# Kernel optimization log

Measured on AMD Instinct MI355X. Metric: run time of the kernel, lower is better.

## Reference

```python
import jax, jax.numpy as jnp
import numpy as np

N = 50000          # nodes (ogbn-products-like subgraph)
E = 800000         # directed edges (avg degree 16)
F_IN, HID, HEADS, OUT = 100, 32, 4, 47
W1 = HID * HEADS   # 128
NEG_SLOPE = 0.2
BN_EPS = 1e-5


def _gatv2(x, src, dst, w_src, w_dst, att, bias, heads, ch):
    """GATv2Conv (PyG semantics, share_weights=False, concat).
    x: [N, F]; src/dst: [Etot] (self-loops already appended);
    w_src/w_dst: [F, heads*ch]; att: [heads, ch]; bias: [heads*ch].
    """
    n = x.shape[0]
    xl = (x @ w_src).reshape(n, heads, ch)   # source-side transform
    xr = (x @ w_dst).reshape(n, heads, ch)   # target-side transform
    # per-edge attention logits: a . leaky_relu(xl[j] + xr[i])  -> [E, heads]
    e = jnp.sum(jax.nn.leaky_relu(xl[src] + xr[dst], NEG_SLOPE) * att, axis=-1)
    # segment softmax over incoming edges of each destination node
    m = jax.ops.segment_max(e, dst, num_segments=n)          # [N, heads]
    ex = jnp.exp(e - m[dst])
    denom = jax.ops.segment_sum(ex, dst, num_segments=n)     # [N, heads]
    alpha = ex / denom[dst]                                  # [E, heads]
    # weighted scatter-add aggregation of source features
    out = jax.ops.segment_sum(alpha[:, :, None] * xl[src], dst, num_segments=n)
    return out.reshape(n, heads * ch) + bias


def _bn_eval(x, g, b, m, v):
    return (x - m) * jax.lax.rsqrt(v + BN_EPS) * g + b


def setup_inputs() -> dict:
    key = jax.random.key(0)
    ks = jax.random.split(key, 32)
    s = 0.1
    inp = {
        "x": jax.random.normal(ks[0], (N, F_IN), jnp.float32),
        "edge_index": jax.random.randint(ks[1], (2, E), 0, N, dtype=jnp.int32),
        "w1_src": jax.random.normal(ks[2], (F_IN, W1), jnp.float32) * s,
        "w1_dst": jax.random.normal(ks[3], (F_IN, W1), jnp.float32) * s,
        "att1": jax.random.normal(ks[4], (HEADS, HID), jnp.float32) * s,
        "b1": jnp.zeros((W1,), jnp.float32),
        "bn1_g": jnp.ones((W1,), jnp.float32),
        "bn1_b": jnp.zeros((W1,), jnp.float32),
        "bn1_m": jax.random.normal(ks[5], (W1,), jnp.float32) * 0.05,
        "bn1_v": jax.random.uniform(ks[6], (W1,), jnp.float32, 0.5, 1.5),
        "res0_w": jax.random.normal(ks[7], (F_IN, W1), jnp.float32) * s,
        "res0_b": jnp.zeros((W1,), jnp.float32),
        "w2_src": jax.random.normal(ks[8], (W1, W1), jnp.float32) * s,
        "w2_dst": jax.random.normal(ks[9], (W1, W1), jnp.float32) * s,
        "att2": jax.random.normal(ks[10], (HEADS, HID), jnp.float32) * s,
        "b2": jnp.zeros((W1,), jnp.float32),
        "bn2_g": jnp.ones((W1,), jnp.float32),
        "bn2_b": jnp.zeros((W1,), jnp.float32),
        "bn2_m": jax.random.normal(ks[11], (W1,), jnp.float32) * 0.05,
        "bn2_v": jax.random.uniform(ks[12], (W1,), jnp.float32, 0.5, 1.5),
        # layer 3: 128 -> 47, heads=1
        "w3_src": jax.random.normal(ks[13], (W1, OUT), jnp.float32) * s,
        "w3_dst": jax.random.normal(ks[14], (W1, OUT), jnp.float32) * s,
        "att3": jax.random.normal(ks[15], (1, OUT), jnp.float32) * s,
        "b3": jnp.zeros((OUT,), jnp.float32),
        "bn3_g": jnp.ones((OUT,), jnp.float32),
        "bn3_b": jnp.zeros((OUT,), jnp.float32),
        "bn3_m": jax.random.normal(ks[16], (OUT,), jnp.float32) * 0.05,
        "bn3_v": jax.random.uniform(ks[17], (OUT,), jnp.float32, 0.5, 1.5),
        "res2_w": jax.random.normal(ks[18], (W1, OUT), jnp.float32) * s,
        "res2_b": jnp.zeros((OUT,), jnp.float32),
    }
    return inp


def reference(x, edge_index,
              w1_src, w1_dst, att1, b1, bn1_g, bn1_b, bn1_m, bn1_v, res0_w, res0_b,
              w2_src, w2_dst, att2, b2, bn2_g, bn2_b, bn2_m, bn2_v,
              w3_src, w3_dst, att3, b3, bn3_g, bn3_b, bn3_m, bn3_v, res2_w, res2_b):
    # add self-loops (PyG GATv2Conv default add_self_loops=True)
    loops = jnp.arange(x.shape[0], dtype=edge_index.dtype)
    src = jnp.concatenate([edge_index[0], loops])
    dst = jnp.concatenate([edge_index[1], loops])

    # layer 1 + linear residual + BN + relu (eval mode: no dropout)
    h = _gatv2(x, src, dst, w1_src, w1_dst, att1, b1, HEADS, HID)
    h = h + (x @ res0_w + res0_b)
    h = jax.nn.relu(_bn_eval(h, bn1_g, bn1_b, bn1_m, bn1_v))

    # layer 2 + identity residual + BN + relu
    h2 = _gatv2(h, src, dst, w2_src, w2_dst, att2, b2, HEADS, HID)
    h2 = h2 + h
    h2 = jax.nn.relu(_bn_eval(h2, bn2_g, bn2_b, bn2_m, bn2_v))

    # layer 3 (heads=1) + linear residual + BN (no relu/dropout on last layer)
    out = _gatv2(h2, src, dst, w3_src, w3_dst, att3, b3, 1, OUT)
    out = out + (h2 @ res2_w + res2_b)
    out = _bn_eval(out, bn3_g, bn3_b, bn3_m, bn3_v)
    return out
```

## Files before the change

### kernel.cpp

```cpp
#include <hip/hip_runtime.h>
#include <math.h>

#define BN_EPS 1e-5f
#define SLOT 96
#define LN16 2.7725887f
#define BCAP 5120

typedef _Float16 h2 __attribute__((ext_vector_type(2)));
typedef _Float16 h4 __attribute__((ext_vector_type(4)));
typedef _Float16 h8 __attribute__((ext_vector_type(8)));
typedef float f2v __attribute__((ext_vector_type(2)));
typedef float float4v __attribute__((ext_vector_type(4)));

static __device__ inline h2 bit_h2(unsigned u) {
    union { unsigned u; h2 h; } c; c.u = u; return c.h;
}
static __device__ inline unsigned bit_u(h2 h) {
    union { unsigned u; h2 h; } c; c.h = h; return c.u;
}

template <int CTRL>
static __device__ inline float dpp_add(float x) {
    int y = __builtin_amdgcn_update_dpp(0, __float_as_int(x), CTRL, 0xF, 0xF, true);
    return x + __int_as_float(y);
}
static __device__ inline float red8_dpp(float t) {
    t = dpp_add<0xB1>(t); t = dpp_add<0x4E>(t); t = dpp_add<0x141>(t);
    return t;
}
static __device__ inline float red16_dpp(float t) {
    t = dpp_add<0xB1>(t); t = dpp_add<0x4E>(t); t = dpp_add<0x141>(t);
    t = dpp_add<0x140>(t);
    return t;
}

static __device__ inline void pack_one(int idx,
                                       const float* p0, const float* p1,
                                       const float* p2,
                                       int w0, int w1, int w2,
                                       int Ksrc, int Ncat,
                                       _Float16* out) {
    int k = idx / Ncat, n = idx - k * Ncat;
    float v = 0.f;
    if (k < Ksrc) {
        if (n < w0) v = p0[(size_t)k * w0 + n];
        else if (n < w0 + w1) v = p1[(size_t)k * w1 + (n - w0)];
        else if (w2 > 0 && n < w0 + w1 + w2) v = p2[(size_t)k * w2 + (n - w0 - w1)];
    }
    int kt = k >> 5, kr = k & 31;
    int quad = kr >> 3, j = kr & 7;
    int nt = n >> 4, nr = n & 15;
    int ntiles = Ncat >> 4;
    out[((size_t)(kt * ntiles + nt) * 64 + quad * 16 + nr) * 8 + j] = (_Float16)v;
}

__global__ __launch_bounds__(256) void prep_bin_k(
    const int* __restrict__ src, const int* __restrict__ dst, int E, int Etot,
    int* __restrict__ gcnt, int* __restrict__ bbuf, int nbA,
    const float* __restrict__ x, _Float16* __restrict__ A, int N,
    const float* __restrict__ w1s, const float* __restrict__ w1d,
    const float* __restrict__ r0w, const float* __restrict__ w2s,
    const float* __restrict__ w2d, const float* __restrict__ w3s,
    const float* __restrict__ w3d, const float* __restrict__ r2w,
    _Float16* __restrict__ Wb1, _Float16* __restrict__ Wb2,
    _Float16* __restrict__ Wb3) {
    if ((int)blockIdx.x < nbA) {
        __shared__ int hist[256];
        __shared__ int base[256];
        int tid = threadIdx.x;
        hist[tid] = 0;
        __syncthreads();
        int per = (Etot + nbA - 1) / nbA;
        int e0 = blockIdx.x * per;
        int e1 = min(e0 + per, Etot);
        for (int i = e0 + tid; i < e1; i += 256) {
            int d = (i < E) ? dst[i] : (i - E);
            atomicAdd(&hist[d >> 8], 1);
        }
        __syncthreads();
        int h = hist[tid];
        if (h) base[tid] = atomicAdd(&gcnt[tid], h);
        __syncthreads();
        for (int i = e0 + tid; i < e1; i += 256) {
            int d = (i < E) ? dst[i] : (i - E);
            int s = (i < E) ? src[i] : (i - E);
            int b = d >> 8;
            int off = atomicAdd(&base[b], 1);
            if (off < BCAP) bbuf[(size_t)b * BCAP + off] = ((d & 255) << 16) | s;
        }
        return;
    }
    const int S1 = 128 * 384, S2 = 128 * 256, S3 = 128 * 144;
    int convTot = N * 32;
    int idx = (blockIdx.x - nbA) * 256 + threadIdx.x;
    if (idx < convTot) {
        int n = idx >> 5, t = idx & 31;
        float4 v = {0.f, 0.f, 0.f, 0.f};
        if (t < 25) v = *(const float4*)(x + (size_t)n * 100 + t * 4);
        h4 o = {(_Float16)v.x, (_Float16)v.y, (_Float16)v.z, (_Float16)v.w};
        *(h4*)(A + (size_t)n * 128 + t * 4) = o;
        return;
    }
    int p = idx - convTot;
    if (p < S1) pack_one(p, w1s, w1d, r0w, 128, 128, 128, 100, 384, Wb1);
    else if (p < S1 + S2) pack_one(p - S1, w2s, w2d, nullptr, 128, 128, 0, 128, 256, Wb2);
    else if (p < S1 + S2 + S3) pack_one(p - S1 - S2, w3s, w3d, r2w, 47, 47, 47, 128, 144, Wb3);
}

template <int NT>
__global__ __launch_bounds__(256) void mfma_gemm(const _Float16* __restrict__ A,
                                                 const _Float16* __restrict__ Bp,
                                                 _Float16* __restrict__ XLR,
                                                 float* __restrict__ RES,
                                                 int M, int Ncat,
                                                 int ncat_valid, int res_off,
                                                 int bf_remap, int bf_shift,
                                                 int bf_stride, int res_stride,
                                                 const int* __restrict__ gcnt,
                                                 const int* __restrict__ bbuf,
                                                 int* __restrict__ esrc,
                                                 int* __restrict__ cnt,
                                                 int scatN, int Nn) {
    __shared__ int lcnt[256];
    int bid = blockIdx.x;
    if (bid < scatN) {
        int tid = threadIdx.x;
        lcnt[tid] = 0;
        __syncthreads();
        int cb = gcnt[bid];
        if (cb > BCAP) cb = BCAP;
        const int* bp = bbuf + (size_t)bid * BCAP;
        int b0 = bid << 8;
        for (int i = tid; i < cb; i += 256) {
            int w = bp[i];
            int dl = (w >> 16) & 255;
            int s = w & 0xFFFF;
            int pos = atomicAdd(&lcnt[dl], 1);
            esrc[(size_t)(b0 + dl) * SLOT + pos] = s << 9;
        }
        __syncthreads();
        int d = b0 + tid;
        if (d < Nn) cnt[d] = lcnt[tid];
        return;
    }
    int mt = ((bid - scatN) * 256 + threadIdx.x) >> 6;
    int lane = threadIdx.x & 63;
    int mtiles = M >> 4;
    if (mt >= mtiles) return;
    int ngroups = Ncat / (16 * NT);
    int ntiles = Ncat >> 4;
    int quad = lane >> 4;
    int nr = lane & 15;
    int row = mt * 16 + nr;

    h8 a[4];
#pragma unroll
    for (int kt = 0; kt < 4; kt++)
        a[kt] = *(const h8*)(A + (size_t)row * 128 + kt * 32 + quad * 8);

    int rowb = mt * 16 + quad * 4;
    for (int ng = 0; ng < ngroups; ng++) {
        float4v acc[NT];
#pragma unroll
        for (int t = 0; t < NT; t++) acc[t] = (float4v){0.f, 0.f, 0.f, 0.f};
#pragma unroll
        for (int kt = 0; kt < 4; kt++) {
            const _Float16* bbase =
                Bp + ((size_t)(kt * ntiles + ng * NT) * 64 + lane) * 8;
#pragma unroll
            for (int t = 0; t < NT; t++) {
                h8 b = *(const h8*)(bbase + (size_t)t * 512);
                acc[t] = __builtin_amdgcn_mfma_f32_16x16x32_f16(a[kt], b, acc[t], 0, 0, 0);
            }
        }
#pragma unroll
        for (int t = 0; t < NT; t++) {
            int col = (ng * NT + t) * 16 + nr;
            if (col >= ncat_valid) continue;
            if (col < res_off) {
                int bc = (col >= bf_remap) ? col + bf_shift : col;
#pragma unroll
                for (int r = 0; r < 4; r++)
                    XLR[(size_t)(rowb + r) * bf_stride + bc] = (_Float16)acc[t][r];
            } else {
                int rc = col - res_off;
#pragma unroll
                for (int r = 0; r < 4; r++)
                    RES[(size_t)(rowb + r) * res_stride + rc] = acc[t][r];
            }
        }
    }
}

static __device__ inline void edge8(uint2 u, h2 xr01, h2 xr23, h2 at01,
                                    h2 at23, float& den, h2& acc01, h2& acc23,
                                    float gate) {
    const h2 NS = {(_Float16)0.2f, (_Float16)0.2f};
    h2 a01 = bit_h2(u.x), a23 = bit_h2(u.y);
    h2 v01 = a01 + xr01, v23 = a23 + xr23;
    v01 = __builtin_elementwise_max(v01, v01 * NS);
    v23 = __builtin_elementwise_max(v23, v23 * NS);
    h2 t2 = v01 * at01 + v23 * at23;
    f2v tf = __builtin_convertvector(t2, f2v);
    float t = red8_dpp(tf.x + tf.y);
    float p = __expf(t - LN16) * gate;
    den += p;
    h2 P = {(_Float16)p, (_Float16)p};
    acc01 = P * a01 + acc01;
    acc23 = P * a23 + acc23;
}
static __device__ inline void edge16(uint2 u, h2 xr01, h2 xr23, h2 at01,
                                     h2 at23, float& den, h2& acc01,
                                     h2& acc23, float gate) {
    const h2 NS = {(_Float16)0.2f, (_Float16)0.2f};
    h2 a01 = bit_h2(u.x), a23 = bit_h2(u.y);
    h2 v01 = a01 + xr01, v23 = a23 + xr23;
    v01 = __builtin_elementwise_max(v01, v01 * NS);
    v23 = __builtin_elementwise_max(v23, v23 * NS);
    h2 t2 = v01 * at01 + v23 * at23;
    f2v tf = __builtin_convertvector(t2, f2v);
    float t = red16_dpp(tf.x + tf.y);
    float p = __expf(t - LN16) * gate;
    den += p;
    h2 P = {(_Float16)p, (_Float16)p};
    acc01 = P * a01 + acc01;
    acc23 = P * a23 + acc23;
}

__global__ __launch_bounds__(256) void gat_agg4_fused(
    const int* __restrict__ cnt, const int* __restrict__ esrc,
    const _Float16* __restrict__ xlr, const float* __restrict__ att,
    const float* __restrict__ RES, const float* __restrict__ resB,
    const float* __restrict__ bias,
    const float* __restrict__ g, const float* __restrict__ bb,
    const float* __restrict__ mm, const float* __restrict__ vv,
    _Float16* __restrict__ hbf, int N, int mode) {
    int d = blockIdx.x * 4 + (threadIdx.x >> 6);
    if (d >= N) return;
    int lane = threadIdx.x & 63;
    int half = lane >> 5;
    int gl = lane & 31;
    int c0 = gl * 4;
    const char* xb = (const char*)xlr + c0 * 2;

    int beg = d * SLOT;
    int cnt_d = cnt[d];
    int myoff = esrc[beg + lane];

    uint2 xrv = *(const uint2*)(xb + (size_t)d * 512 + 256);
    float4 af = *(const float4*)(att + c0);
    float4 rres = {0.f, 0.f, 0.f, 0.f};
    uint2 hprev = {0u, 0u};
    if (mode == 1) rres = *(const float4*)(RES + (size_t)d * 128 + c0);
    else hprev = *(const uint2*)(hbf + (size_t)d * 128 + c0);
    float4 bi = *(const float4*)(bias + c0);

    h2 xr01 = bit_h2(xrv.x), xr23 = bit_h2(xrv.y);
    h2 at01 = {(_Float16)af.x, (_Float16)af.y};
    h2 at23 = {(_Float16)af.z, (_Float16)af.w};

    int K = (cnt_d + 1) >> 1;
    int KB = K < 12 ? K : 12;
    uint2 u[12];
#pragma unroll
    for (int k = 0; k < 12; k++) {
        if (k < KB) {
            int ee = 2 * k + half;
            int ec = ee < cnt_d ? ee : 0;
            int o = __shfl(myoff, ec);
            u[k] = *(const uint2*)(xb + o);
        }
    }
    float den = 0.f;
    h2 acc01 = {(_Float16)0.f, (_Float16)0.f};
    h2 acc23 = acc01;
#pragma unroll
    for (int k = 0; k < 12; k++) {
        if (k < KB) {
            int ee = 2 * k + half;
            edge8(u[k], xr01, xr23, at01, at23, den, acc01, acc23,
                  ee < cnt_d ? 1.f : 0.f);
        }
    }
    for (int e = 24; e < cnt_d; e += 2) {
        int ee = e + half;
        bool act = ee < cnt_d;
        int ec = act ? ee : cnt_d - 1;
        int o = __shfl(myoff, ec < 64 ? ec : 0);
        if (ec >= 64) o = esrc[beg + ec];
        uint2 u0 = *(const uint2*)(xb + o);
        edge8(u0, xr01, xr23, at01, at23, den, acc01, acc23, act ? 1.f : 0.f);
    }
    den += __shfl_xor(den, 32);
    f2v c01 = __builtin_convertvector(acc01, f2v);
    f2v c23 = __builtin_convertvector(acc23, f2v);
    float f0 = c01.x, f1 = c01.y, fA = c23.x, fB = c23.y;
    f0 += __shfl_xor(f0, 32);
    f1 += __shfl_xor(f1, 32);
    fA += __shfl_xor(fA, 32);
    fB += __shfl_xor(fB, 32);

    if (half == 0) {
        float inv = 1.f / den;
        float o0 = f0 * inv + bi.x;
        float o1 = f1 * inv + bi.y;
        float o2 = fA * inv + bi.z;
        float o3 = fB * inv + bi.w;
        if (mode == 1) {
            float4 rb = *(const float4*)(resB + c0);
            o0 += rres.x + rb.x; o1 += rres.y + rb.y;
            o2 += rres.z + rb.z; o3 += rres.w + rb.w;
        } else {
            f2v g01 = __builtin_convertvector(bit_h2(hprev.x), f2v);
            f2v g23 = __builtin_convertvector(bit_h2(hprev.y), f2v);
            o0 += g01.x; o1 += g01.y; o2 += g23.x; o3 += g23.y;
        }
        float4 gm = *(const float4*)(mm + c0);
        float4 gv = *(const float4*)(vv + c0);
        float4 gg = *(const float4*)(g + c0);
        float4 gb = *(const float4*)(bb + c0);
        o0 = fmaxf((o0 - gm.x) * rsqrtf(gv.x + BN_EPS) * gg.x + gb.x, 0.f);
        o1 = fmaxf((o1 - gm.y) * rsqrtf(gv.y + BN_EPS) * gg.y + gb.y, 0.f);
        o2 = fmaxf((o2 - gm.z) * rsqrtf(gv.z + BN_EPS) * gg.z + gb.z, 0.f);
        o3 = fmaxf((o3 - gm.w) * rsqrtf(gv.w + BN_EPS) * gg.w + gb.w, 0.f);
        h2 s01 = {(_Float16)o0, (_Float16)o1};
        h2 s23 = {(_Float16)o2, (_Float16)o3};
        uint2 w;
        w.x = bit_u(s01);
        w.y = bit_u(s23);
        *(uint2*)(hbf + (size_t)d * 128 + c0) = w;
    }
}

__global__ __launch_bounds__(256) void gat_agg1_fused(
    const int* __restrict__ cnt, const int* __restrict__ esrc,
    const _Float16* __restrict__ xlr, const float* __restrict__ att,
    const float* __restrict__ RES, const float* __restrict__ resB,
    const float* __restrict__ bias,
    const float* __restrict__ g, const float* __restrict__ bb,
    const float* __restrict__ mm, const float* __restrict__ vv,
    float* __restrict__ out, int N) {
    int d = blockIdx.x * 4 + (threadIdx.x >> 6);
    if (d >= N) return;
    int lane = threadIdx.x & 63;
    int gl = lane & 15, grp = lane >> 4;
    const char* xb = (const char*)xlr + gl * 8;

    int beg = d * SLOT;
    int cnt_d = cnt[d];
    int myoff = esrc[beg + lane] >> 1;

    uint2 xrv = *(const uint2*)(xb + (size_t)d * 256 + 128);
    float4 rres = *(const float4*)(RES + (size_t)d * 48 + gl * 4);

    h2 xr01 = bit_h2(xrv.x), xr23 = bit_h2(xrv.y);
    float atf[4];
#pragma unroll
    for (int k = 0; k < 4; k++) {
        int c = gl * 4 + k;
        atf[k] = (c < 47) ? att[c] : 0.f;
    }
    h2 at01 = {(_Float16)atf[0], (_Float16)atf[1]};
    h2 at23 = {(_Float16)atf[2], (_Float16)atf[3]};

    int nmain = cnt_d < 64 ? cnt_d : 64;
    int nb1 = nmain < 48 ? nmain : 48;
    int K1 = (nb1 + 3) >> 2;
    uint2 u[12];
#pragma unroll
    for (int k = 0; k < 12; k++) {
        if (k < K1) {
            int idx = grp + 4 * k;
            int ec = idx < nmain ? idx : 0;
            int o = __shfl(myoff, ec);
            u[k] = *(const uint2*)(xb + o);
        }
    }
    float den = 0.f;
    h2 acc01 = {(_Float16)0.f, (_Float16)0.f};
    h2 acc23 = acc01;
#pragma unroll
    for (int k = 0; k < 12; k++) {
        if (k < K1) {
            int idx = grp + 4 * k;
            edge16(u[k], xr01, xr23, at01, at23, den, acc01, acc23,
                   idx < nmain ? 1.f : 0.f);
        }
    }
    for (int ibase = 48; ibase < nmain; ibase += 4) {
        int idx = ibase + grp;
        bool act = idx < nmain;
        int o = __shfl(myoff, act ? idx : 0);
        uint2 u0 = *(const uint2*)(xb + o);
        edge16(u0, xr01, xr23, at01, at23, den, acc01, acc23, act ? 1.f : 0.f);
    }
    for (int j = beg + 64 + grp; j < beg + cnt_d; j += 4) {
        int o = esrc[j] >> 1;
        uint2 u0 = *(const uint2*)(xb + o);
        edge16(u0, xr01, xr23, at01, at23, den, acc01, acc23, 1.f);
    }
    den += __shfl_xor(den, 16);
    den += __shfl_xor(den, 32);
    f2v c01 = __builtin_convertvector(acc01, f2v);
    f2v c23 = __builtin_convertvector(acc23, f2v);
    float f[4] = {c01.x, c01.y, c23.x, c23.y};
#pragma unroll
    for (int k = 0; k < 4; k++) {
        f[k] += __shfl_xor(f[k], 16);
        f[k] += __shfl_xor(f[k], 32);
    }
    if (grp == 0 && gl < 12) {
        float inv = 1.f / den;
        float rr[4] = {rres.x, rres.y, rres.z, rres.w};
#pragma unroll
        for (int k = 0; k < 4; k++) {
            int c = gl * 4 + k;
            if (c < 47) {
                float o = f[k] * inv + bias[c] + rr[k] + resB[c];
                o = (o - mm[c]) * rsqrtf(vv[c] + BN_EPS) * g[c] + bb[c];
                out[(size_t)d * 47 + c] = o;
            }
        }
    }
}

extern "C" void kernel_launch(void* const* d_in, const int* in_sizes, int n_in,
                              void* d_out, int out_size, void* d_ws, size_t ws_size,
                              hipStream_t stream) {
    const float* x      = (const float*)d_in[0];
    const int*   ei     = (const int*)d_in[1];
    const float* w1_src = (const float*)d_in[2];
    const float* w1_dst = (const float*)d_in[3];
    const float* att1   = (const float*)d_in[4];
    const float* b1     = (const float*)d_in[5];
    const float* bn1_g  = (const float*)d_in[6];
    const float* bn1_b  = (const float*)d_in[7];
    const float* bn1_m  = (const float*)d_in[8];
    const float* bn1_v  = (const float*)d_in[9];
    const float* res0_w = (const float*)d_in[10];
    const float* res0_b = (const float*)d_in[11];
    const float* w2_src = (const float*)d_in[12];
    const float* w2_dst = (const float*)d_in[13];
    const float* att2   = (const float*)d_in[14];
    const float* b2     = (const float*)d_in[15];
    const float* bn2_g  = (const float*)d_in[16];
    const float* bn2_b  = (const float*)d_in[17];
    const float* bn2_m  = (const float*)d_in[18];
    const float* bn2_v  = (const float*)d_in[19];
    const float* w3_src = (const float*)d_in[20];
    const float* w3_dst = (const float*)d_in[21];
    const float* att3   = (const float*)d_in[22];
    const float* b3     = (const float*)d_in[23];
    const float* bn3_g  = (const float*)d_in[24];
    const float* bn3_b  = (const float*)d_in[25];
    const float* bn3_m  = (const float*)d_in[26];
    const float* bn3_v  = (const float*)d_in[27];
    const float* res2_w = (const float*)d_in[28];
    const float* res2_b = (const float*)d_in[29];

    const int F_IN = 100;
    const int KP = 128;
    const int NC1 = 384, NC2 = 256, NC3 = 144;
    int N = in_sizes[0] / F_IN;
    int E = in_sizes[1] / 2;
    int Etot = E + N;
    const int* src = ei;
    const int* dst = ei + E;
    int nbuck = (N + 255) >> 8;

    float* ws = (float*)d_ws;
    size_t o = 0;
    _Float16* XLR = (_Float16*)(ws + o); o += (size_t)N * 128;
    float* B_res = ws + o; o += (size_t)N * 128;
    _Float16* A_h = (_Float16*)(ws + o); o += (size_t)N * 64;
    _Float16* Wb1 = (_Float16*)(ws + o); o += (size_t)KP * NC1 / 2;
    _Float16* Wb2 = (_Float16*)(ws + o); o += (size_t)KP * NC2 / 2;
    _Float16* Wb3 = (_Float16*)(ws + o); o += (size_t)KP * NC3 / 2;
    int* I_cnt  = (int*)(ws + o); o += N;
    int* I_esrc = (int*)(ws + o); o += (size_t)N * SLOT + 4;
    int* I_gcnt = (int*)(ws + o); o += 256;
    int* I_bbuf = (int*)(ws + o); o += (size_t)nbuck * BCAP;
    (void)ws_size; (void)n_in; (void)out_size;

    int mtiles = (N + 15) / 16;
    int aggGrid = (N + 3) / 4;
    int gemmGrid = (mtiles + 3) / 4;

    hipMemsetAsync(I_gcnt, 0, 256 * sizeof(int), stream);

    {
        int nbA = 512;
        int convTot = N * 32;
        int packTot = KP * (NC1 + NC2 + NC3);
        int pb = (convTot + packTot + 255) / 256;
        prep_bin_k<<<nbA + pb, 256, 0, stream>>>(
            src, dst, E, Etot, I_gcnt, I_bbuf, nbA, x, A_h, N,
            w1_src, w1_dst, res0_w, w2_src, w2_dst, w3_src, w3_dst, res2_w,
            Wb1, Wb2, Wb3);
    }

    mfma_gemm<4><<<nbuck + gemmGrid, 256, 0, stream>>>(
        A_h, Wb1, XLR, B_res, N, NC1, 384, 256, 384, 0, 256, 128,
        I_gcnt, I_bbuf, I_esrc, I_cnt, nbuck, N);
    gat_agg4_fused<<<aggGrid, 256, 0, stream>>>(
        I_cnt, I_esrc, XLR, att1, B_res, res0_b, b1,
        bn1_g, bn1_b, bn1_m, bn1_v, A_h, N, 1);

    mfma_gemm<4><<<gemmGrid, 256, 0, stream>>>(
        A_h, Wb2, XLR, B_res, N, NC2, 256, 256, 256, 0, 256, 128,
        nullptr, nullptr, nullptr, nullptr, 0, N);
    gat_agg4_fused<<<aggGrid, 256, 0, stream>>>(
        I_cnt, I_esrc, XLR, att2, nullptr, nullptr, b2,
        bn2_g, bn2_b, bn2_m, bn2_v, A_h, N, 2);

    mfma_gemm<3><<<gemmGrid, 256, 0, stream>>>(
        A_h, Wb3, XLR, B_res, N, NC3, 141, 94, 47, 17, 128, 48,
        nullptr, nullptr, nullptr, nullptr, 0, N);
    gat_agg1_fused<<<aggGrid, 256, 0, stream>>>(
        I_cnt, I_esrc, XLR, att3, B_res, res2_b, b3,
        bn3_g, bn3_b, bn3_m, bn3_v, (float*)d_out, N);
}
```

Before: 326.0 us.

## Fuse next-layer MFMA GEMM into GAT aggregation kernels via shared-memory tile

The aggregation kernel now processes 16 nodes per block (4 per wave), stages the normalized fp16 outputs in a shared-memory tile, and then runs the next layer's MFMA projection directly on that tile. This removes the separate GEMM launches for layers 2 and 3 and the global round trip of the hidden activations. Buffers are ping-ponged between XLR and B_res, and the layer-3 layout changes to a 512-byte stride with the residual interleaved. Each wave now handles nodes serially and the block adds a sync, so gather latency hiding per wave may drop, and the B-matrix fragments are reloaded by every block.

```diff
diff --git a/kernel.cpp b/kernel.cpp
--- a/kernel.cpp
+++ b/kernel.cpp
@@ -227,108 +227,172 @@
     acc23 = P * a23 + acc23;
 }
 
-__global__ __launch_bounds__(256) void gat_agg4_fused(
+__global__ __launch_bounds__(256) void gat_agg4_gemm(
     const int* __restrict__ cnt, const int* __restrict__ esrc,
-    const _Float16* __restrict__ xlr, const float* __restrict__ att,
-    const float* __restrict__ RES, const float* __restrict__ resB,
-    const float* __restrict__ bias,
+    const _Float16* __restrict__ xlr,
+    const float* __restrict__ att,
+    const float* __restrict__ RES,
+    const _Float16* __restrict__ hprev,
+    const float* __restrict__ resB, const float* __restrict__ bias,
     const float* __restrict__ g, const float* __restrict__ bb,
     const float* __restrict__ mm, const float* __restrict__ vv,
-    _Float16* __restrict__ hbf, int N, int mode) {
-    int d = blockIdx.x * 4 + (threadIdx.x >> 6);
-    if (d >= N) return;
+    _Float16* __restrict__ hout,
+    const _Float16* __restrict__ Bp,
+    _Float16* __restrict__ XLRo, float* __restrict__ RESo,
+    int Ncat, int ncat_valid, int res_off, int bf_remap, int bf_shift,
+    int bf_stride, int res_stride,
+    int N, int mode) {
+    __shared__ _Float16 hT[16][136];
+    int d0 = blockIdx.x * 16;
+    int wv = threadIdx.x >> 6;
     int lane = threadIdx.x & 63;
     int half = lane >> 5;
     int gl = lane & 31;
     int c0 = gl * 4;
     const char* xb = (const char*)xlr + c0 * 2;
 
-    int beg = d * SLOT;
-    int cnt_d = cnt[d];
-    int myoff = esrc[beg + lane];
-
-    uint2 xrv = *(const uint2*)(xb + (size_t)d * 512 + 256);
     float4 af = *(const float4*)(att + c0);
-    float4 rres = {0.f, 0.f, 0.f, 0.f};
-    uint2 hprev = {0u, 0u};
-    if (mode == 1) rres = *(const float4*)(RES + (size_t)d * 128 + c0);
-    else hprev = *(const uint2*)(hbf + (size_t)d * 128 + c0);
-    float4 bi = *(const float4*)(bias + c0);
-
-    h2 xr01 = bit_h2(xrv.x), xr23 = bit_h2(xrv.y);
     h2 at01 = {(_Float16)af.x, (_Float16)af.y};
     h2 at23 = {(_Float16)af.z, (_Float16)af.w};
-
-    int K = (cnt_d + 1) >> 1;
-    int KB = K < 12 ? K : 12;
-    uint2 u[12];
-#pragma unroll
-    for (int k = 0; k < 12; k++) {
-        if (k < KB) {
-            int ee = 2 * k + half;
-            int ec = ee < cnt_d ? ee : 0;
-            int o = __shfl(myoff, ec);
-            u[k] = *(const uint2*)(xb + o);
-        }
-    }
-    float den = 0.f;
-    h2 acc01 = {(_Float16)0.f, (_Float16)0.f};
-    h2 acc23 = acc01;
-#pragma unroll
-    for (int k = 0; k < 12; k++) {
-        if (k < KB) {
-            int ee = 2 * k + half;
-            edge8(u[k], xr01, xr23, at01, at23, den, acc01, acc23,
-                  ee < cnt_d ? 1.f : 0.f);
-        }
-    }
-    for (int e = 24; e < cnt_d; e += 2) {
-        int ee = e + half;
-        bool act = ee < cnt_d;
-        int ec = act ? ee : cnt_d - 1;
-        int o = __shfl(myoff, ec < 64 ? ec : 0);
-        if (ec >= 64) o = esrc[beg + ec];
-        uint2 u0 = *(const uint2*)(xb + o);
-        edge8(u0, xr01, xr23, at01, at23, den, acc01, acc23, act ? 1.f : 0.f);
-    }
-    den += __shfl_xor(den, 32);
-    f2v c01 = __builtin_convertvector(acc01, f2v);
-    f2v c23 = __builtin_convertvector(acc23, f2v);
-    float f0 = c01.x, f1 = c01.y, fA = c23.x, fB = c23.y;
-    f0 += __shfl_xor(f0, 32);
-    f1 += __shfl_xor(f1, 32);
-    fA += __shfl_xor(fA, 32);
-    fB += __shfl_xor(fB, 32);
-
-    if (half == 0) {
-        float inv = 1.f / den;
-        float o0 = f0 * inv + bi.x;
-        float o1 = f1 * inv + bi.y;
-        float o2 = fA * inv + bi.z;
-        float o3 = fB * inv + bi.w;
-        if (mode == 1) {
-            float4 rb = *(const float4*)(resB + c0);
-            o0 += rres.x + rb.x; o1 += rres.y + rb.y;
-            o2 += rres.z + rb.z; o3 += rres.w + rb.w;
+    float4 bi = *(const float4*)(bias + c0);
+    float4 gm = *(const float4*)(mm + c0);
+    float4 gv = *(const float4*)(vv + c0);
+    float4 gg = *(const float4*)(g + c0);
+    float4 gb = *(const float4*)(bb + c0);
+    float4 rb = {0.f, 0.f, 0.f, 0.f};
+    if (mode == 1) rb = *(const float4*)(resB + c0);
+
+    int myoff4[4], cnt4[4];
+#pragma unroll
+    for (int i = 0; i < 4; i++) {
+        int dd = d0 + (wv << 2) + i;
+        dd = dd < N ? dd : N - 1;
+        cnt4[i] = cnt[dd];
+        myoff4[i] = esrc[(size_t)dd * SLOT + lane];
+    }
+
+#pragma unroll
+    for (int i = 0; i < 4; i++) {
+        int d = d0 + (wv << 2) + i;
+        int dd = d < N ? d : N - 1;
+        int beg = dd * SLOT;
+        int cnt_d = cnt4[i];
+        int myoff = myoff4[i];
+
+        uint2 xrv = *(const uint2*)(xb + (size_t)dd * 512 + 256);
+        h2 xr01 = bit_h2(xrv.x), xr23 = bit_h2(xrv.y);
+        float4 rres = {0.f, 0.f, 0.f, 0.f};
+        uint2 hpv = {0u, 0u};
+        if (mode == 1) rres = *(const float4*)(RES + (size_t)dd * 128 + c0);
+        else hpv = *(const uint2*)(hprev + (size_t)dd * 128 + c0);
+
+        int K = (cnt_d + 1) >> 1;
+        int KB = K < 12 ? K : 12;
+        uint2 u[12];
+#pragma unroll
+        for (int k = 0; k < 12; k++) {
+            if (k < KB) {
+                int ee = 2 * k + half;
+                int ec = ee < cnt_d ? ee : 0;
+                int o = __shfl(myoff, ec);
+                u[k] = *(const uint2*)(xb + o);
+            }
+        }
+        float den = 0.f;
+        h2 acc01 = {(_Float16)0.f, (_Float16)0.f};
+        h2 acc23 = acc01;
+#pragma unroll
+        for (int k = 0; k < 12; k++) {
+            if (k < KB) {
+                int ee = 2 * k + half;
+                edge8(u[k], xr01, xr23, at01, at23, den, acc01, acc23,
+                      ee < cnt_d ? 1.f : 0.f);
+            }
+        }
+        for (int e = 24; e < cnt_d; e += 2) {
+            int ee = e + half;
+            bool act = ee < cnt_d;
+            int ec = act ? ee : cnt_d - 1;
+            int o = __shfl(myoff, ec < 64 ? ec : 0);
+            if (ec >= 64) o = esrc[beg + ec];
+            uint2 u0 = *(const uint2*)(xb + o);
+            edge8(u0, xr01, xr23, at01, at23, den, acc01, acc23,
+                  act ? 1.f : 0.f);
+        }
+        den += __shfl_xor(den, 32);
+        f2v c01 = __builtin_convertvector(acc01, f2v);
+        f2v c23 = __builtin_convertvector(acc23, f2v);
+        float f0 = c01.x, f1 = c01.y, fA = c23.x, fB = c23.y;
+        f0 += __shfl_xor(f0, 32);
+        f1 += __shfl_xor(f1, 32);
+        fA += __shfl_xor(fA, 32);
+        fB += __shfl_xor(fB, 32);
+
+        if (half == 0) {
+            float inv = 1.f / den;
+            float o0 = f0 * inv + bi.x;
+            float o1 = f1 * inv + bi.y;
+            float o2 = fA * inv + bi.z;
+            float o3 = fB * inv + bi.w;
+            if (mode == 1) {
+                o0 += rres.x + rb.x; o1 += rres.y + rb.y;
+                o2 += rres.z + rb.z; o3 += rres.w + rb.w;
+            } else {
+                f2v g01 = __builtin_convertvector(bit_h2(hpv.x), f2v);
+                f2v g23 = __builtin_convertvector(bit_h2(hpv.y), f2v);
+                o0 += g01.x; o1 += g01.y; o2 += g23.x; o3 += g23.y;
+            }
+            o0 = fmaxf((o0 - gm.x) * rsqrtf(gv.x + BN_EPS) * gg.x + gb.x, 0.f);
+            o1 = fmaxf((o1 - gm.y) * rsqrtf(gv.y + BN_EPS) * gg.y + gb.y, 0.f);
+            o2 = fmaxf((o2 - gm.z) * rsqrtf(gv.z + BN_EPS) * gg.z + gb.z, 0.f);
+            o3 = fmaxf((o3 - gm.w) * rsqrtf(gv.w + BN_EPS) * gg.w + gb.w, 0.f);
+            h2 s01 = {(_Float16)o0, (_Float16)o1};
+            h2 s23 = {(_Float16)o2, (_Float16)o3};
+            uint2 w;
+            w.x = bit_u(s01);
+            w.y = bit_u(s23);
+            int lr = (wv << 2) + i;
+            *(uint2*)(&hT[lr][c0]) = w;
+            if (mode == 1 && d < N)
+                *(uint2*)(hout + (size_t)d * 128 + c0) = w;
+        }
+    }
+    __syncthreads();
+
+    int quad = lane >> 4;
+    int nr = lane & 15;
+    h8 a[4];
+#pragma unroll
+    for (int kt = 0; kt < 4; kt++)
+        a[kt] = *(const h8*)(&hT[nr][kt * 32 + quad * 8]);
+
+    int ntiles = Ncat >> 4;
+    for (int t = wv; t < ntiles; t += 4) {
+        float4v acc = (float4v){0.f, 0.f, 0.f, 0.f};
+#pragma unroll
+        for (int kt = 0; kt < 4; kt++) {
+            h8 b = *(const h8*)(Bp + ((size_t)(kt * ntiles + t) * 64 + lane) * 8);
+            acc = __builtin_amdgcn_mfma_f32_16x16x32_f16(a[kt], b, acc, 0, 0, 0);
+        }
+        int col = t * 16 + nr;
+        if (col >= ncat_valid) continue;
+        if (col < res_off) {
+            int bc = (col >= bf_remap) ? col + bf_shift : col;
+#pragma unroll
+            for (int r = 0; r < 4; r++) {
+                int grow = d0 + quad * 4 + r;
+                if (grow < N)
+                    XLRo[(size_t)grow * bf_stride + bc] = (_Float16)acc[r];
+            }
         } else {
-            f2v g01 = __builtin_convertvector(bit_h2(hprev.x), f2v);
-            f2v g23 = __builtin_convertvector(bit_h2(hprev.y), f2v);
-            o0 += g01.x; o1 += g01.y; o2 += g23.x; o3 += g23.y;
-        }
-        float4 gm = *(const float4*)(mm + c0);
-        float4 gv = *(const float4*)(vv + c0);
-        float4 gg = *(const float4*)(g + c0);
-        float4 gb = *(const float4*)(bb + c0);
-        o0 = fmaxf((o0 - gm.x) * rsqrtf(gv.x + BN_EPS) * gg.x + gb.x, 0.f);
-        o1 = fmaxf((o1 - gm.y) * rsqrtf(gv.y + BN_EPS) * gg.y + gb.y, 0.f);
-        o2 = fmaxf((o2 - gm.z) * rsqrtf(gv.z + BN_EPS) * gg.z + gb.z, 0.f);
-        o3 = fmaxf((o3 - gm.w) * rsqrtf(gv.w + BN_EPS) * gg.w + gb.w, 0.f);
-        h2 s01 = {(_Float16)o0, (_Float16)o1};
-        h2 s23 = {(_Float16)o2, (_Float16)o3};
-        uint2 w;
-        w.x = bit_u(s01);
-        w.y = bit_u(s23);
-        *(uint2*)(hbf + (size_t)d * 128 + c0) = w;
+            int rc = col - res_off;
+#pragma unroll
+            for (int r = 0; r < 4; r++) {
+                int grow = d0 + quad * 4 + r;
+                if (grow < N)
+                    RESo[(size_t)grow * res_stride + rc] = acc[r];
+            }
+        }
     }
 }
 
@@ -348,10 +412,10 @@
 
     int beg = d * SLOT;
     int cnt_d = cnt[d];
-    int myoff = esrc[beg + lane] >> 1;
-
-    uint2 xrv = *(const uint2*)(xb + (size_t)d * 256 + 128);
-    float4 rres = *(const float4*)(RES + (size_t)d * 48 + gl * 4);
+    int myoff = esrc[beg + lane];
+
+    uint2 xrv = *(const uint2*)(xb + (size_t)d * 512 + 128);
+    float4 rres = *(const float4*)(RES + (size_t)d * 128 + gl * 4);
 
     h2 xr01 = bit_h2(xrv.x), xr23 = bit_h2(xrv.y);
     float atf[4];
@@ -395,7 +459,7 @@
         edge16(u0, xr01, xr23, at01, at23, den, acc01, acc23, act ? 1.f : 0.f);
     }
     for (int j = beg + 64 + grp; j < beg + cnt_d; j += 4) {
-        int o = esrc[j] >> 1;
+        int o = esrc[j];
         uint2 u0 = *(const uint2*)(xb + o);
         edge16(u0, xr01, xr23, at01, at23, den, acc01, acc23, 1.f);
     }
@@ -483,6 +547,7 @@
     (void)ws_size; (void)n_in; (void)out_size;
 
     int mtiles = (N + 15) / 16;
+    int agg16Grid = (N + 15) / 16;
     int aggGrid = (N + 3) / 4;
     int gemmGrid = (mtiles + 3) / 4;
 
@@ -502,21 +567,22 @@
     mfma_gemm<4><<<nbuck + gemmGrid, 256, 0, stream>>>(
         A_h, Wb1, XLR, B_res, N, NC1, 384, 256, 384, 0, 256, 128,
         I_gcnt, I_bbuf, I_esrc, I_cnt, nbuck, N);
-    gat_agg4_fused<<<aggGrid, 256, 0, stream>>>(
-        I_cnt, I_esrc, XLR, att1, B_res, res0_b, b1,
-        bn1_g, bn1_b, bn1_m, bn1_v, A_h, N, 1);
-
-    mfma_gemm<4><<<gemmGrid, 256, 0, stream>>>(
-        A_h, Wb2, XLR, B_res, N, NC2, 256, 256, 256, 0, 256, 128,
-        nullptr, nullptr, nullptr, nullptr, 0, N);
-    gat_agg4_fused<<<aggGrid, 256, 0, stream>>>(
-        I_cnt, I_esrc, XLR, att2, nullptr, nullptr, b2,
-        bn2_g, bn2_b, bn2_m, bn2_v, A_h, N, 2);
-
-    mfma_gemm<3><<<gemmGrid, 256, 0, stream>>>(
-        A_h, Wb3, XLR, B_res, N, NC3, 141, 94, 47, 17, 128, 48,
-        nullptr, nullptr, nullptr, nullptr, 0, N);
+
+    gat_agg4_gemm<<<agg16Grid, 256, 0, stream>>>(
+        I_cnt, I_esrc, XLR, att1, B_res, nullptr, res0_b, b1,
+        bn1_g, bn1_b, bn1_m, bn1_v, A_h,
+        Wb2, (_Float16*)B_res, nullptr,
+        NC2, 256, 256, 384, 0, 256, 0,
+        N, 1);
+
+    gat_agg4_gemm<<<agg16Grid, 256, 0, stream>>>(
+        I_cnt, I_esrc, (const _Float16*)B_res, att2, nullptr, A_h, nullptr, b2,
+        bn2_g, bn2_b, bn2_m, bn2_v, nullptr,
+        Wb3, XLR, (float*)XLR + 64,
+        NC3, 141, 94, 47, 17, 256, 128,
+        N, 2);
+
     gat_agg1_fused<<<aggGrid, 256, 0, stream>>>(
-        I_cnt, I_esrc, XLR, att3, B_res, res2_b, b3,
+        I_cnt, I_esrc, XLR, att3, (const float*)((float*)XLR + 64), res2_b, b3,
         bn3_g, bn3_b, bn3_m, bn3_v, (float*)d_out, N);
 }
```

After: 327.5 us. Within noise of the previous version (+0.4%).
